# Optimization experiments

Hardware: AMD Instinct MI355X
Metric: run time of the kernel (lower is better)

Reference implementation:

```python
import jax, jax.numpy as jnp
import numpy as np

N_NODES = 100000
N_EDGES = 2000000


def _init_mlp(key, dims, scale=0.05):
    Ws, bs = [], []
    ks = jax.random.split(key, len(dims) - 1)
    for k, di, do in zip(ks, dims[:-1], dims[1:]):
        Ws.append(jax.random.normal(k, (di, do), dtype=jnp.float32) * scale)
        bs.append(jnp.zeros((do,), dtype=jnp.float32))
    return Ws, bs


def setup_inputs() -> dict:
    key = jax.random.key(0)
    ks = jax.random.split(key, 7)
    d = {
        "t": jax.random.uniform(ks[0], (1,), dtype=jnp.float32),
        "x": jax.random.normal(ks[1], (N_NODES, 4), dtype=jnp.float32),
        "Ofixed": jax.random.normal(ks[2], (N_NODES, 2), dtype=jnp.float32),
        "src_idx": jax.random.randint(ks[3], (N_EDGES,), 0, N_NODES, dtype=jnp.int32),
        "tgt_idx": jax.random.randint(ks[4], (N_EDGES,), 0, N_NODES, dtype=jnp.int32),
    }
    # fR: (2*d_O+1)=13 -> [150]*4 -> 50 ; fO: 50 -> [100] -> 4
    R_Ws, R_bs = _init_mlp(ks[5], [13, 150, 150, 150, 150, 50])
    O_Ws, O_bs = _init_mlp(ks[6], [50, 100, 4])
    for i, (W, b) in enumerate(zip(R_Ws, R_bs)):
        d[f"fR_W{i}"] = W
        d[f"fR_b{i}"] = b
    for i, (W, b) in enumerate(zip(O_Ws, O_bs)):
        d[f"fO_W{i}"] = W
        d[f"fO_b{i}"] = b
    return d


def _mlp(h, Ws, bs):
    # hidden layers with ReLU, linear output (matches MLP in the torch code)
    for W, b in zip(Ws[:-1], bs[:-1]):
        h = jax.nn.relu(h @ W + b)
    return h @ Ws[-1] + bs[-1]


def reference(t, x, Ofixed, src_idx, tgt_idx,
              fR_W0, fR_b0, fR_W1, fR_b1, fR_W2, fR_b2, fR_W3, fR_b3, fR_W4, fR_b4,
              fO_W0, fO_b0, fO_W1, fO_b1):
    O = jnp.concatenate([x, Ofixed], axis=1)            # [N, d_O]
    # Msrc.T @ O and Mtgt.T @ O with 0/1 incidence matrices == gathers
    Rsrc = O[src_idx]                                   # [M, d_O]
    Rtgt = O[tgt_idx]                                   # [M, d_O]
    tt = jnp.broadcast_to(t.reshape(1, 1).astype(O.dtype), (src_idx.shape[0], 1))
    R_prime = jnp.concatenate([Rsrc, Rtgt, tt], axis=1)  # [M, 2*d_O+1]
    E = _mlp(R_prime, [fR_W0, fR_W1, fR_W2, fR_W3, fR_W4],
             [fR_b0, fR_b1, fR_b2, fR_b3, fR_b4])        # [M, d_E]
    # Mtgt @ E == scatter-add of edge messages onto target nodes
    E_prime = jax.ops.segment_sum(E, tgt_idx, num_segments=x.shape[0])  # [N, d_E]
    P = _mlp(E_prime, [fO_W0, fO_W1], [fO_b0, fO_b1])    # [N, d_P]
    return P
```

## Files before the change

kernel.cpp:

```cpp
#include <hip/hip_runtime.h>
#include <hip/hip_bf16.h>

typedef unsigned short u16;
typedef unsigned int u32;
typedef __attribute__((ext_vector_type(8))) short short8;
typedef __attribute__((ext_vector_type(4))) float f32x4;

constexpr int SA     = 168;
constexpr int BLK_E  = 64;
constexpr int NTHR   = 256;
constexpr int CHUNK  = 512;
constexpr int WSLOT  = 50 * CHUNK;
constexpr size_t WS_HDR   = 262144;

constexpr int Ls (int s) { return s == 0 ? 0 : (s <= 15 ? 1 + (s - 1) / 5 : 4); }
constexpr int Kss(int s) { return s == 0 ? 0 : (s <= 15 ? (s - 1) % 5 : s - 16); }

__device__ __forceinline__ u16 f2bf(float f) {
    union { float f; unsigned u; } c; c.f = f;
    return (u16)((c.u + 0x7fffu + ((c.u >> 16) & 1u)) >> 16);
}
__device__ __forceinline__ unsigned pk_bf16(float a, float b) {
    float2 f; f.x = a; f.y = b;
    __hip_bfloat162 h = __float22bfloat162_rn(f);
    return *(unsigned*)&h;
}

__device__ __forceinline__ int kperm(int kp) {
    if (kp < 64)  return (kp & 3) * 16 + (kp >> 2);
    if (kp < 128) { const int m = kp - 64; return (5 + (m & 3)) * 16 + (m >> 2); }
    if (kp < 144) return 4 * 16 + (kp - 128);
    if (kp < 160) return 9 * 16 + (kp - 144);
    return 1 << 30;
}

__global__ void prep_all(const float* __restrict__ W0, const float* __restrict__ W1,
                         const float* __restrict__ W2, const float* __restrict__ W3,
                         const float* __restrict__ W4,
                         const float* __restrict__ B0, const float* __restrict__ B1,
                         const float* __restrict__ B2, const float* __restrict__ B3,
                         const float* __restrict__ B4,
                         u16* __restrict__ Wt)
{
    const int l = blockIdx.y;
    const float* W; const float* B; int DI, DO; bool perm;
    if      (l == 0) { W = W0; B = B0; DI = 13;  DO = 150; perm = false; }
    else if (l == 1) { W = W1; B = B1; DI = 150; DO = 150; perm = true;  }
    else if (l == 2) { W = W2; B = B2; DI = 150; DO = 150; perm = true;  }
    else if (l == 3) { W = W3; B = B3; DI = 150; DO = 150; perm = true;  }
    else             { W = W4; B = B4; DI = 150; DO = 50;  perm = true;  }
    const int kbias = (l == 0) ? 13 : 150;
    u16* dst = Wt + (size_t)l * WSLOT;
    for (int idx = blockIdx.x * blockDim.x + threadIdx.x; idx < WSLOT;
         idx += gridDim.x * blockDim.x) {
        const int chunk = idx / CHUNK;
        const int within = idx - chunk * CHUNK;
        const int lane = within >> 3, e = within & 7;
        const int ks = chunk / 10, j = chunk - ks * 10;
        const int c = lane & 15, q = lane >> 4;
        const int n = j * 16 + c;
        const int kphys = ks * 32 + q * 8 + e;
        const int klog = perm ? kperm(kphys) : kphys;
        float v = 0.f;
        if (n < DO) {
            if (klog < DI)          v = W[klog * DO + n];
            else if (klog == kbias) v = B[n];
        }
        dst[idx] = f2bf(v);
    }
}

__device__ __forceinline__ void loadB(const u16* __restrict__ Wt, int s,
                                      int ng, int lane, short8 (&slot)[5])
{
    const int l = Ls(s), ks = Kss(s);
    const int jb = (l < 4) ? ng * 5 : 0;
    const int nt = (l < 4) ? 5 : 4;
    const u16* base = Wt + (size_t)l * WSLOT + (size_t)(ks * 10 + jb) * CHUNK + lane * 8;
#pragma unroll
    for (int jj = 0; jj < 5; ++jj)
        if (jj < nt) slot[jj] = *(const short8*)&base[jj * CHUNK];
}

__device__ __forceinline__ void epilogue(u16* act, int mg, int ng, int col, int quad,
                                         f32x4 (&acc)[2][5])
{
#pragma unroll
    for (int mtl = 0; mtl < 2; ++mtl)
#pragma unroll
        for (int r = 0; r < 4; ++r) {
            u16* row = &act[((mg * 2 + mtl) * 16 + quad * 4 + r) * SA];
            uint2 pk;
            pk.x = pk_bf16(fmaxf(acc[mtl][0][r], 0.f), fmaxf(acc[mtl][1][r], 0.f));
            pk.y = pk_bf16(fmaxf(acc[mtl][2][r], 0.f), fmaxf(acc[mtl][3][r], 0.f));
            *(uint2*)&row[ng * 64 + col * 4] = pk;
            u16 sv = (u16)pk_bf16(fmaxf(acc[mtl][4][r], 0.f), 0.f);
            if (ng == 1 && col == 6) sv = 0x3F80;
            row[128 + ng * 16 + col] = sv;
        }
}

__global__ void hist_kernel(const int* __restrict__ tgt, u32* __restrict__ cnt,
                            int n_edges)
{
    const int e = blockIdx.x * blockDim.x + threadIdx.x;
    if (e < n_edges) atomicAdd(&cnt[tgt[e]], 1u);
}

__global__ void scan1_kernel(const u32* __restrict__ cnt, u32* __restrict__ offs,
                             u32* __restrict__ bsum, int n)
{
    __shared__ u32 s[256];
    const int i = blockIdx.x * 256 + threadIdx.x;
    const u32 v = (i < n) ? cnt[i] : 0u;
    s[threadIdx.x] = v; __syncthreads();
#pragma unroll
    for (int d = 1; d < 256; d <<= 1) {
        const u32 t = (threadIdx.x >= d) ? s[threadIdx.x - d] : 0u;
        __syncthreads();
        s[threadIdx.x] += t;
        __syncthreads();
    }
    if (i < n) offs[i] = s[threadIdx.x] - v;
    if (threadIdx.x == 255) bsum[blockIdx.x] = s[255];
}

__global__ void scan2_kernel(u32* __restrict__ bsum, int nb)
{
    __shared__ u32 s[512];
    const int i = threadIdx.x;
    const u32 v = (i < nb) ? bsum[i] : 0u;
    s[i] = v; __syncthreads();
#pragma unroll
    for (int d = 1; d < 512; d <<= 1) {
        const u32 t = (i >= d) ? s[i - d] : 0u;
        __syncthreads();
        s[i] += t;
        __syncthreads();
    }
    if (i < nb) bsum[i] = s[i] - v;
}

__global__ void scan3_kernel(u32* __restrict__ offs, const u32* __restrict__ bsum,
                             u32* __restrict__ cursor, int n, int n_edges)
{
    const int i = blockIdx.x * 256 + threadIdx.x;
    if (i < n) {
        const u32 o = offs[i] + bsum[blockIdx.x];
        offs[i] = o;
        cursor[i] = o;
    }
    if (blockIdx.x == 0 && threadIdx.x == 0) offs[n] = (u32)n_edges;
}

__global__ void perm_kernel(const int* __restrict__ src, const int* __restrict__ tgt,
                            u32* __restrict__ cursor,
                            int* __restrict__ src_perm, int* __restrict__ tgt_perm,
                            int n_edges)
{
    const int e = blockIdx.x * blockDim.x + threadIdx.x;
    if (e < n_edges) {
        const int g = tgt[e];
        const u32 pos = atomicAdd(&cursor[g], 1u);
        src_perm[pos] = src[e];
        tgt_perm[pos] = g;
    }
}

__global__ __launch_bounds__(NTHR, 4) void edge_kernel(
    const float* __restrict__ t, const float* __restrict__ x, const float* __restrict__ Ofx,
    const int* __restrict__ src, const int* __restrict__ tgt,
    const u16* __restrict__ Wt,
    float* __restrict__ Ep, int n_edges)
{
    __shared__ __align__(16) u16 act[BLK_E * SA];
    __shared__ int tgt_s[BLK_E];

    const int tid  = threadIdx.x;
    const int lane = tid & 63;
    const int wv   = tid >> 6;
    const int mg   = wv >> 1;
    const int ng   = wv & 1;
    const int col  = lane & 15;
    const int quad = lane >> 4;

    short8 Bwin[3][5];
    loadB(Wt, 0, ng, lane, Bwin[0]);
    loadB(Wt, 1, ng, lane, Bwin[1]);
    loadB(Wt, 2, ng, lane, Bwin[2]);

    if (tid < BLK_E) {
        const int e = tid;
        const long long ge = (long long)blockIdx.x * BLK_E + e;
        const bool valid = ge < n_edges;
        const int s = valid ? src[ge] : 0;
        const int g = valid ? tgt[ge] : 0;
        const float4 xs = valid ? *(const float4*)&x[(size_t)s * 4] : float4{0, 0, 0, 0};
        const float2 os = valid ? *(const float2*)&Ofx[(size_t)s * 2] : float2{0, 0};
        const float4 xg = valid ? *(const float4*)&x[(size_t)g * 4] : float4{0, 0, 0, 0};
        const float2 og = valid ? *(const float2*)&Ofx[(size_t)g * 2] : float2{0, 0};
        const float tv = valid ? t[0] : 0.f;
        uint4 w0, w1;
        w0.x = pk_bf16(xs.x, xs.y); w0.y = pk_bf16(xs.z, xs.w);
        w0.z = pk_bf16(os.x, os.y); w0.w = pk_bf16(xg.x, xg.y);
        w1.x = pk_bf16(xg.z, xg.w); w1.y = pk_bf16(og.x, og.y);
        w1.z = pk_bf16(tv, 1.0f);   w1.w = 0u;
        u16* row = &act[e * SA];
        *(uint4*)&row[0]  = w0;
        *(uint4*)&row[8]  = w1;
        *(uint4*)&row[16] = uint4{0, 0, 0, 0};
        *(uint4*)&row[24] = uint4{0, 0, 0, 0};
        tgt_s[e] = valid ? g : -1;
    }
    __syncthreads();

    f32x4 acc[2][5];
    short8 Af[2];

#pragma unroll
    for (int mtl = 0; mtl < 2; ++mtl)
#pragma unroll
        for (int jj = 0; jj < 5; ++jj) acc[mtl][jj] = f32x4{0.f, 0.f, 0.f, 0.f};
#pragma unroll
    for (int mtl = 0; mtl < 2; ++mtl)
        Af[mtl] = *(const short8*)&act[((mg * 2 + mtl) * 16 + col) * SA + quad * 8];
#pragma unroll
    for (int jj = 0; jj < 5; ++jj)
#pragma unroll
        for (int mtl = 0; mtl < 2; ++mtl)
            acc[mtl][jj] = __builtin_amdgcn_mfma_f32_16x16x32_bf16(
                Af[mtl], Bwin[0][jj], acc[mtl][jj], 0, 0, 0);
    loadB(Wt, 3, ng, lane, Bwin[0]);
    __syncthreads();
    epilogue(act, mg, ng, col, quad, acc);
    __syncthreads();

#pragma unroll
    for (int s = 1; s <= 15; ++s) {
        const int ks = (s - 1) % 5;
        const int slot = s % 3;
        if (ks == 0) {
#pragma unroll
            for (int mtl = 0; mtl < 2; ++mtl)
#pragma unroll
                for (int jj = 0; jj < 5; ++jj) acc[mtl][jj] = f32x4{0.f, 0.f, 0.f, 0.f};
        }
#pragma unroll
        for (int mtl = 0; mtl < 2; ++mtl)
            Af[mtl] = *(const short8*)&act[((mg * 2 + mtl) * 16 + col) * SA
                                           + ks * 32 + quad * 8];
#pragma unroll
        for (int jj = 0; jj < 5; ++jj)
#pragma unroll
            for (int mtl = 0; mtl < 2; ++mtl)
                acc[mtl][jj] = __builtin_amdgcn_mfma_f32_16x16x32_bf16(
                    Af[mtl], Bwin[slot][jj], acc[mtl][jj], 0, 0, 0);
        if (s + 3 <= 20) loadB(Wt, s + 3, ng, lane, Bwin[slot]);
        if (ks == 4) {
            __syncthreads();
            epilogue(act, mg, ng, col, quad, acc);
            __syncthreads();
        }
    }

    const int mt4 = mg * 2 + ng;
    f32x4 acc4[4];
#pragma unroll
    for (int jj = 0; jj < 4; ++jj) acc4[jj] = f32x4{0.f, 0.f, 0.f, 0.f};
#pragma unroll
    for (int s = 16; s <= 20; ++s) {
        const int ks = s - 16;
        const int slot = s % 3;
        const short8 A4 = *(const short8*)&act[(mt4 * 16 + col) * SA
                                               + ks * 32 + quad * 8];
#pragma unroll
        for (int jj = 0; jj < 4; ++jj)
            acc4[jj] = __builtin_amdgcn_mfma_f32_16x16x32_bf16(
                A4, Bwin[slot][jj], acc4[jj], 0, 0, 0);
        if (s + 3 <= 20) loadB(Wt, s + 3, ng, lane, Bwin[slot]);
    }

    __syncthreads();
    float* actF = (float*)act;
#pragma unroll
    for (int jj = 0; jj < 4; ++jj) {
        const int n = jj * 16 + col;
        if (n < 50) {
#pragma unroll
            for (int r = 0; r < 4; ++r)
                actF[(mt4 * 16 + quad * 4 + r) * 52 + n] = acc4[jj][r];
        }
    }
    __syncthreads();
    if (tid < 100) {
        const int h = tid / 50;
        const int c = tid - h * 50;
        int   cur = tgt_s[h * 32];
        float a   = 0.f;
        for (int r = h * 32; r < h * 32 + 32; ++r) {
            const int   g = tgt_s[r];
            const float v = actF[r * 52 + c];
            if (g != cur) {
                if (cur >= 0) atomicAdd(&Ep[(size_t)cur * 50 + c], a);
                a = 0.f; cur = g;
            }
            a += v;
        }
        if (cur >= 0) atomicAdd(&Ep[(size_t)cur * 50 + c], a);
    }
}

template<int DI, int DO, bool RELU>
__device__ __forceinline__ void mlp_layer_t(
    const float* __restrict__ W, const float* __restrict__ B,
    float (*in)[64], float (*out)[64], int tid)
{
    const int et = tid & 15;
    const int jt = tid >> 4;
    constexpr int NG = (DO + 15) / 16;

    float acc0[NG], acc1[NG], acc2[NG], acc3[NG];
#pragma unroll
    for (int g = 0; g < NG; ++g) {
        const int j = jt + 16 * g;
        const float bb = (j < DO) ? B[j] : 0.f;
        acc0[g] = bb; acc1[g] = bb; acc2[g] = bb; acc3[g] = bb;
    }
    for (int k = 0; k < DI; ++k) {
        const float4 a = *(const float4*)&in[k][et * 4];
#pragma unroll
        for (int g = 0; g < NG; ++g) {
            const int j = jt + 16 * g;
            const float wv = (j < DO) ? W[k * DO + j] : 0.f;
            acc0[g] = fmaf(a.x, wv, acc0[g]);
            acc1[g] = fmaf(a.y, wv, acc1[g]);
            acc2[g] = fmaf(a.z, wv, acc2[g]);
            acc3[g] = fmaf(a.w, wv, acc3[g]);
        }
    }
#pragma unroll
    for (int g = 0; g < NG; ++g) {
        const int j = jt + 16 * g;
        if (j < DO) {
            float4 v; v.x = acc0[g]; v.y = acc1[g]; v.z = acc2[g]; v.w = acc3[g];
            if (RELU) {
                v.x = fmaxf(v.x, 0.f); v.y = fmaxf(v.y, 0.f);
                v.z = fmaxf(v.z, 0.f); v.w = fmaxf(v.w, 0.f);
            }
            *(float4*)&out[j][et * 4] = v;
        }
    }
}

__global__ __launch_bounds__(256, 2) void node_kernel(
    const float* __restrict__ Ep, int ncopies, size_t copy_elems,
    const float* __restrict__ W0, const float* __restrict__ B0,
    const float* __restrict__ W1, const float* __restrict__ B1,
    float* __restrict__ P, int n_nodes)
{
    __shared__ float bufA[104][64];
    __shared__ float bufB[104][64];
    const int tid = threadIdx.x;
    const int n0  = blockIdx.x * 64;

    for (int idx = tid; idx < 64 * 50; idx += 256) {
        const int e = idx / 50;
        const int k = idx - e * 50;
        const int n = n0 + e;
        float s = 0.f;
        if (n < n_nodes) {
            const float* p = &Ep[(size_t)n * 50 + k];
            for (int c = 0; c < ncopies; ++c) s += p[(size_t)c * copy_elems];
        }
        bufA[k][e] = s;
    }
    __syncthreads();
    mlp_layer_t<50, 100, true >(W0, B0, bufA, bufB, tid); __syncthreads();
    mlp_layer_t<100, 4, false>(W1, B1, bufB, bufA, tid); __syncthreads();
    for (int idx = tid; idx < 64 * 4; idx += 256) {
        const int e = idx & 63;
        const int j = idx >> 6;
        const int n = n0 + e;
        if (n < n_nodes) P[(size_t)n * 4 + j] = bufA[j][e];
    }
}

extern "C" void kernel_launch(void* const* d_in, const int* in_sizes, int n_in,
                              void* d_out, int out_size, void* d_ws, size_t ws_size,
                              hipStream_t stream)
{
    const float* t   = (const float*)d_in[0];
    const float* x   = (const float*)d_in[1];
    const float* Ofx = (const float*)d_in[2];
    const int*   src = (const int*)d_in[3];
    const int*   tgt = (const int*)d_in[4];
    const float* W0  = (const float*)d_in[5];  const float* B0 = (const float*)d_in[6];
    const float* W1  = (const float*)d_in[7];  const float* B1 = (const float*)d_in[8];
    const float* W2  = (const float*)d_in[9];  const float* B2 = (const float*)d_in[10];
    const float* W3  = (const float*)d_in[11]; const float* B3 = (const float*)d_in[12];
    const float* W4  = (const float*)d_in[13]; const float* B4 = (const float*)d_in[14];
    const float* OW0 = (const float*)d_in[15]; const float* OB0 = (const float*)d_in[16];
    const float* OW1 = (const float*)d_in[17]; const float* OB1 = (const float*)d_in[18];

    const int n_nodes = in_sizes[1] / 4;
    const int n_edges = in_sizes[3];

    auto align256 = [](size_t v) { return (v + 255) & ~(size_t)255; };
    char* ws = (char*)d_ws;
    const size_t copy_elems = (size_t)n_nodes * 50;
    size_t o = 0;
    u16*   Wt       = (u16*)(ws + o);  o = WS_HDR;
    float* Ep       = (float*)(ws + o); o = align256(o + copy_elems * sizeof(float));
    u32*   offs     = (u32*)(ws + o);  o = align256(o + (size_t)(n_nodes + 1) * 4);
    u32*   cursor   = (u32*)(ws + o);  o = align256(o + (size_t)n_nodes * 4);
    u32*   bsum     = (u32*)(ws + o);  o = align256(o + 512 * 4);
    int*   src_perm = (int*)(ws + o);  o = align256(o + (size_t)n_edges * 4);
    int*   tgt_perm = (int*)(ws + o);  o = align256(o + (size_t)n_edges * 4);

    const int NB  = (n_nodes + 255) / 256;
    const int EBK = (n_edges + 255) / 256;

    prep_all<<<dim3(32, 5), 256, 0, stream>>>(W0, W1, W2, W3, W4,
                                              B0, B1, B2, B3, B4, Wt);
    hipMemsetAsync(Ep, 0, copy_elems * sizeof(float), stream);
    hipMemsetAsync(cursor, 0, (size_t)n_nodes * 4, stream);

    hist_kernel <<<EBK, 256, 0, stream>>>(tgt, cursor, n_edges);
    scan1_kernel<<<NB, 256, 0, stream>>>(cursor, offs, bsum, n_nodes);
    scan2_kernel<<<1, 512, 0, stream>>>(bsum, NB);
    scan3_kernel<<<NB, 256, 0, stream>>>(offs, bsum, cursor, n_nodes, n_edges);
    perm_kernel <<<EBK, 256, 0, stream>>>(src, tgt, cursor, src_perm, tgt_perm, n_edges);

    edge_kernel<<<(n_edges + BLK_E - 1) / BLK_E, NTHR, 0, stream>>>(
        t, x, Ofx, src_perm, tgt_perm, Wt, Ep, n_edges);

    node_kernel<<<(n_nodes + 63) / 64, 256, 0, stream>>>(
        Ep, 1, copy_elems, OW0, OB0, OW1, OB1, (float*)d_out, n_nodes);
}
```

Before: 872.1 us.

## Pack permuted src/tgt into int2, spread gather across waves, widen segmented reduction

The permute kernel now writes source and target indices as one interleaved int2 array, so the edge kernel reads one 8-byte value per edge instead of two separate arrays. The edge gather is spread over 16 lanes of each of the four waves instead of the first 64 threads. The per-block segmented scatter-add uses 200 threads over 16-row spans instead of 100 threads over 32-row spans. Accumulator zeroing is folded into the first MFMA by passing a zero operand, and the unused multi-copy path in the node kernel is removed. Shorter spans can mean more atomics when a target's run crosses a span boundary.

```diff
diff --git a/kernel.cpp b/kernel.cpp
--- a/kernel.cpp
+++ b/kernel.cpp
@@ -154,22 +154,20 @@
 }
 
 __global__ void perm_kernel(const int* __restrict__ src, const int* __restrict__ tgt,
-                            u32* __restrict__ cursor,
-                            int* __restrict__ src_perm, int* __restrict__ tgt_perm,
+                            u32* __restrict__ cursor, int2* __restrict__ sg,
                             int n_edges)
 {
     const int e = blockIdx.x * blockDim.x + threadIdx.x;
     if (e < n_edges) {
         const int g = tgt[e];
         const u32 pos = atomicAdd(&cursor[g], 1u);
-        src_perm[pos] = src[e];
-        tgt_perm[pos] = g;
+        sg[pos] = make_int2(src[e], g);
     }
 }
 
 __global__ __launch_bounds__(NTHR, 4) void edge_kernel(
     const float* __restrict__ t, const float* __restrict__ x, const float* __restrict__ Ofx,
-    const int* __restrict__ src, const int* __restrict__ tgt,
+    const int2* __restrict__ sgp,
     const u16* __restrict__ Wt,
     float* __restrict__ Ep, int n_edges)
 {
@@ -189,16 +187,17 @@
     loadB(Wt, 1, ng, lane, Bwin[1]);
     loadB(Wt, 2, ng, lane, Bwin[2]);
 
-    if (tid < BLK_E) {
-        const int e = tid;
+    if (lane < 16) {
+        const int e = wv * 16 + lane;
         const long long ge = (long long)blockIdx.x * BLK_E + e;
         const bool valid = ge < n_edges;
-        const int s = valid ? src[ge] : 0;
-        const int g = valid ? tgt[ge] : 0;
+        const int2 sg = valid ? sgp[ge] : make_int2(0, 0);
+        const int s = sg.x;
+        const int g = valid ? sg.y : -1;
         const float4 xs = valid ? *(const float4*)&x[(size_t)s * 4] : float4{0, 0, 0, 0};
         const float2 os = valid ? *(const float2*)&Ofx[(size_t)s * 2] : float2{0, 0};
-        const float4 xg = valid ? *(const float4*)&x[(size_t)g * 4] : float4{0, 0, 0, 0};
-        const float2 og = valid ? *(const float2*)&Ofx[(size_t)g * 2] : float2{0, 0};
+        const float4 xg = valid ? *(const float4*)&x[(size_t)sg.y * 4] : float4{0, 0, 0, 0};
+        const float2 og = valid ? *(const float2*)&Ofx[(size_t)sg.y * 2] : float2{0, 0};
         const float tv = valid ? t[0] : 0.f;
         uint4 w0, w1;
         w0.x = pk_bf16(xs.x, xs.y); w0.y = pk_bf16(xs.z, xs.w);
@@ -210,26 +209,23 @@
         *(uint4*)&row[8]  = w1;
         *(uint4*)&row[16] = uint4{0, 0, 0, 0};
         *(uint4*)&row[24] = uint4{0, 0, 0, 0};
-        tgt_s[e] = valid ? g : -1;
-    }
-    __syncthreads();
-
+        tgt_s[e] = g;
+    }
+    __syncthreads();
+
+    const f32x4 z = {0.f, 0.f, 0.f, 0.f};
     f32x4 acc[2][5];
     short8 Af[2];
 
 #pragma unroll
     for (int mtl = 0; mtl < 2; ++mtl)
-#pragma unroll
-        for (int jj = 0; jj < 5; ++jj) acc[mtl][jj] = f32x4{0.f, 0.f, 0.f, 0.f};
-#pragma unroll
-    for (int mtl = 0; mtl < 2; ++mtl)
         Af[mtl] = *(const short8*)&act[((mg * 2 + mtl) * 16 + col) * SA + quad * 8];
 #pragma unroll
     for (int jj = 0; jj < 5; ++jj)
 #pragma unroll
         for (int mtl = 0; mtl < 2; ++mtl)
             acc[mtl][jj] = __builtin_amdgcn_mfma_f32_16x16x32_bf16(
-                Af[mtl], Bwin[0][jj], acc[mtl][jj], 0, 0, 0);
+                Af[mtl], Bwin[0][jj], z, 0, 0, 0);
     loadB(Wt, 3, ng, lane, Bwin[0]);
     __syncthreads();
     epilogue(act, mg, ng, col, quad, acc);
@@ -239,12 +235,6 @@
     for (int s = 1; s <= 15; ++s) {
         const int ks = (s - 1) % 5;
         const int slot = s % 3;
-        if (ks == 0) {
-#pragma unroll
-            for (int mtl = 0; mtl < 2; ++mtl)
-#pragma unroll
-                for (int jj = 0; jj < 5; ++jj) acc[mtl][jj] = f32x4{0.f, 0.f, 0.f, 0.f};
-        }
 #pragma unroll
         for (int mtl = 0; mtl < 2; ++mtl)
             Af[mtl] = *(const short8*)&act[((mg * 2 + mtl) * 16 + col) * SA
@@ -252,9 +242,14 @@
 #pragma unroll
         for (int jj = 0; jj < 5; ++jj)
 #pragma unroll
-            for (int mtl = 0; mtl < 2; ++mtl)
-                acc[mtl][jj] = __builtin_amdgcn_mfma_f32_16x16x32_bf16(
-                    Af[mtl], Bwin[slot][jj], acc[mtl][jj], 0, 0, 0);
+            for (int mtl = 0; mtl < 2; ++mtl) {
+                if (ks == 0)
+                    acc[mtl][jj] = __builtin_amdgcn_mfma_f32_16x16x32_bf16(
+                        Af[mtl], Bwin[slot][jj], z, 0, 0, 0);
+                else
+                    acc[mtl][jj] = __builtin_amdgcn_mfma_f32_16x16x32_bf16(
+                        Af[mtl], Bwin[slot][jj], acc[mtl][jj], 0, 0, 0);
+            }
         if (s + 3 <= 20) loadB(Wt, s + 3, ng, lane, Bwin[slot]);
         if (ks == 4) {
             __syncthreads();
@@ -266,17 +261,20 @@
     const int mt4 = mg * 2 + ng;
     f32x4 acc4[4];
 #pragma unroll
-    for (int jj = 0; jj < 4; ++jj) acc4[jj] = f32x4{0.f, 0.f, 0.f, 0.f};
-#pragma unroll
     for (int s = 16; s <= 20; ++s) {
         const int ks = s - 16;
         const int slot = s % 3;
         const short8 A4 = *(const short8*)&act[(mt4 * 16 + col) * SA
                                                + ks * 32 + quad * 8];
 #pragma unroll
-        for (int jj = 0; jj < 4; ++jj)
-            acc4[jj] = __builtin_amdgcn_mfma_f32_16x16x32_bf16(
-                A4, Bwin[slot][jj], acc4[jj], 0, 0, 0);
+        for (int jj = 0; jj < 4; ++jj) {
+            if (ks == 0)
+                acc4[jj] = __builtin_amdgcn_mfma_f32_16x16x32_bf16(
+                    A4, Bwin[slot][jj], z, 0, 0, 0);
+            else
+                acc4[jj] = __builtin_amdgcn_mfma_f32_16x16x32_bf16(
+                    A4, Bwin[slot][jj], acc4[jj], 0, 0, 0);
+        }
         if (s + 3 <= 20) loadB(Wt, s + 3, ng, lane, Bwin[slot]);
     }
 
@@ -292,12 +290,13 @@
         }
     }
     __syncthreads();
-    if (tid < 100) {
+    if (tid < 200) {
         const int h = tid / 50;
         const int c = tid - h * 50;
-        int   cur = tgt_s[h * 32];
+        const int r0 = h * 16;
+        int   cur = tgt_s[r0];
         float a   = 0.f;
-        for (int r = h * 32; r < h * 32 + 32; ++r) {
+        for (int r = r0; r < r0 + 16; ++r) {
             const int   g = tgt_s[r];
             const float v = actF[r * 52 + c];
             if (g != cur) {
@@ -353,7 +352,7 @@
 }
 
 __global__ __launch_bounds__(256, 2) void node_kernel(
-    const float* __restrict__ Ep, int ncopies, size_t copy_elems,
+    const float* __restrict__ Ep,
     const float* __restrict__ W0, const float* __restrict__ B0,
     const float* __restrict__ W1, const float* __restrict__ B1,
     float* __restrict__ P, int n_nodes)
@@ -367,12 +366,7 @@
         const int e = idx / 50;
         const int k = idx - e * 50;
         const int n = n0 + e;
-        float s = 0.f;
-        if (n < n_nodes) {
-            const float* p = &Ep[(size_t)n * 50 + k];
-            for (int c = 0; c < ncopies; ++c) s += p[(size_t)c * copy_elems];
-        }
-        bufA[k][e] = s;
+        bufA[k][e] = (n < n_nodes) ? Ep[(size_t)n * 50 + k] : 0.f;
     }
     __syncthreads();
     mlp_layer_t<50, 100, true >(W0, B0, bufA, bufB, tid); __syncthreads();
@@ -414,8 +408,7 @@
     u32*   offs     = (u32*)(ws + o);  o = align256(o + (size_t)(n_nodes + 1) * 4);
     u32*   cursor   = (u32*)(ws + o);  o = align256(o + (size_t)n_nodes * 4);
     u32*   bsum     = (u32*)(ws + o);  o = align256(o + 512 * 4);
-    int*   src_perm = (int*)(ws + o);  o = align256(o + (size_t)n_edges * 4);
-    int*   tgt_perm = (int*)(ws + o);  o = align256(o + (size_t)n_edges * 4);
+    int2*  sg_perm  = (int2*)(ws + o); o = align256(o + (size_t)n_edges * 8);
 
     const int NB  = (n_nodes + 255) / 256;
     const int EBK = (n_edges + 255) / 256;
@@ -429,11 +422,11 @@
     scan1_kernel<<<NB, 256, 0, stream>>>(cursor, offs, bsum, n_nodes);
     scan2_kernel<<<1, 512, 0, stream>>>(bsum, NB);
     scan3_kernel<<<NB, 256, 0, stream>>>(offs, bsum, cursor, n_nodes, n_edges);
-    perm_kernel <<<EBK, 256, 0, stream>>>(src, tgt, cursor, src_perm, tgt_perm, n_edges);
+    perm_kernel <<<EBK, 256, 0, stream>>>(src, tgt, cursor, sg_perm, n_edges);
 
     edge_kernel<<<(n_edges + BLK_E - 1) / BLK_E, NTHR, 0, stream>>>(
-        t, x, Ofx, src_perm, tgt_perm, Wt, Ep, n_edges);
+        t, x, Ofx, sg_perm, Wt, Ep, n_edges);
 
     node_kernel<<<(n_nodes + 63) / 64, 256, 0, stream>>>(
-        Ep, 1, copy_elems, OW0, OB0, OW1, OB1, (float*)d_out, n_nodes);
-}
+        Ep, OW0, OB0, OW1, OB1, (float*)d_out, n_nodes);
+}
```

Measured after the change: 898.4 us. +3.0%, slower.
